# Kernel tuning notes

Hardware: AMD Instinct MI355X
Metric: run time of the kernel (lower is better)

Reference implementation:

```python
import jax, jax.numpy as jnp
import numpy as np

N_NODES = 50000
N_EDGES = 800000
D = 64
N_GRAPHS = 64


def setup_inputs() -> dict:
    key = jax.random.key(0)
    ks = jax.random.split(key, 8)
    scale = 1.0 / np.sqrt(D)
    x = jax.random.normal(ks[0], (N_NODES, D), dtype=jnp.float32)
    edge_index = jax.random.randint(ks[1], (2, N_EDGES), 0, N_NODES, dtype=jnp.int32)
    batch = jnp.sort(jax.random.randint(ks[2], (N_NODES,), 0, N_GRAPHS, dtype=jnp.int32))
    Wq = jax.random.normal(ks[3], (D, D), dtype=jnp.float32) * scale
    Wk = jax.random.normal(ks[4], (D, D), dtype=jnp.float32) * scale
    Wv = jax.random.normal(ks[5], (D, D), dtype=jnp.float32) * scale
    Ws = jax.random.normal(ks[6], (D, D), dtype=jnp.float32) * scale
    z = jnp.zeros((D,), dtype=jnp.float32)
    return {"x": x, "edge_index": edge_index, "batch": batch,
            "Wq": Wq, "bq": z, "Wk": Wk, "bk": z, "Wv": Wv, "bv": z,
            "Ws": Ws, "bs": z}


def reference(x, edge_index, batch, Wq, bq, Wk, bk, Wv, bv, Ws, bs):
    # TransformerConv(heads=1, concat=True, root_weight=True), then ReLU, then global_mean_pool
    src = edge_index[0]  # source node j (message sender)
    dst = edge_index[1]  # target node i (message receiver)
    q = x @ Wq + bq      # [N, D]
    k = x @ Wk + bk      # [N, D]
    v = x @ Wv + bv      # [N, D]
    inv_sqrt_d = jnp.float32(1.0 / np.sqrt(D))
    # per-edge attention logits: (q_i . k_j) / sqrt(D)
    logits = jnp.sum(q[dst] * k[src], axis=-1) * inv_sqrt_d  # [E]
    # segment softmax over incoming edges of each target node
    seg_max = jax.ops.segment_max(logits, dst, num_segments=N_NODES)  # [N]
    ex = jnp.exp(logits - seg_max[dst])                               # [E]
    denom = jax.ops.segment_sum(ex, dst, num_segments=N_NODES)        # [N]
    alpha = ex / denom[dst]                                           # [E]
    # scatter-add weighted values to target nodes
    agg = jax.ops.segment_sum(alpha[:, None] * v[src], dst, num_segments=N_NODES)  # [N, D]
    out = agg + (x @ Ws + bs)  # root/skip connection
    out = jax.nn.relu(out)
    # global mean pool per graph
    sums = jax.ops.segment_sum(out, batch, num_segments=N_GRAPHS)            # [G, D]
    cnt = jax.ops.segment_sum(jnp.ones((N_NODES,), out.dtype), batch, num_segments=N_GRAPHS)
    return sums / jnp.maximum(cnt, 1.0)[:, None]
```

## Files before the change

kernel.cpp:

```cpp
#include <hip/hip_runtime.h>
#include <hip/hip_bf16.h>

#define D 64
#define NG 64
#define CAP 64
#define NB 196
#define BCAP 5120

typedef short bf16x8 __attribute__((ext_vector_type(8)));
typedef float f32x4  __attribute__((ext_vector_type(4)));
typedef unsigned short u16x8 __attribute__((ext_vector_type(8)));

__device__ __forceinline__ float b2f(unsigned short u){
  return __uint_as_float(((unsigned)u) << 16);
}
__device__ __forceinline__ unsigned short f2bu(float f){
  return __builtin_bit_cast(unsigned short, __float2bfloat16(f));
}

template<int C>
__device__ __forceinline__ float dppadd(float x){
  int t = __builtin_amdgcn_update_dpp(0, __float_as_int(x), C, 0xf, 0xf, true);
  return x + __int_as_float(t);
}

__global__ __launch_bounds__(256) void k_wprep(
    const float* __restrict__ Wq, const float* __restrict__ Wk,
    const float* __restrict__ Wv, const float* __restrict__ Ws,
    short* __restrict__ fragw, int* __restrict__ zptr, int zn)
{
  for (int i = blockIdx.x*256 + threadIdx.x; i < zn; i += 8*256) zptr[i] = 0;

  const int m    = blockIdx.x >> 1;
  const int kh   = blockIdx.x & 1;
  const int ct   = threadIdx.x >> 6;
  const int lane = threadIdx.x & 63;
  const int r16  = lane & 15;
  const int kg   = lane >> 4;
  const float* Wm = (m==0) ? Wq : (m==1) ? Wk : (m==2) ? Wv : Ws;
  bf16x8 hi, lo;
  #pragma unroll
  for (int j = 0; j < 8; ++j){
    float wv = Wm[(32*kh + 8*kg + j)*D + 16*ct + r16];
    unsigned short hb = f2bu(wv);
    hi[j] = (short)hb;
    lo[j] = (short)f2bu(wv - b2f(hb));
  }
  int fi = ct*2 + kh;
  *(bf16x8*)(fragw + ((size_t)(fi*2+0)*256 + m*64 + lane)*8) = hi;
  *(bf16x8*)(fragw + ((size_t)(fi*2+1)*256 + m*64 + lane)*8) = lo;
}

__global__ __launch_bounds__(256) void k_split(
    const int* __restrict__ esrc, const int* __restrict__ edst,
    int* __restrict__ bcnt, unsigned* __restrict__ bedge, int E, int nChunk)
{
  __shared__ int hist[NB], gpos[NB], cur[NB];
  const int tid = threadIdx.x;
  if (tid < NB){ hist[tid] = 0; cur[tid] = 0; }
  __syncthreads();
  const int c0 = blockIdx.x * nChunk;
  const int c1 = min(c0 + nChunk, E);
  for (int e = c0 + tid; e < c1; e += 256)
    atomicAdd(&hist[edst[e] >> 8], 1);
  __syncthreads();
  if (tid < NB && hist[tid] > 0)
    gpos[tid] = atomicAdd(bcnt + tid*16, hist[tid]);
  __syncthreads();
  for (int e = c0 + tid; e < c1; e += 256){
    int d = edst[e];
    int b = d >> 8;
    int p = gpos[b] + atomicAdd(&cur[b], 1);
    if (p < BCAP)
      bedge[(size_t)b*BCAP + p] = (unsigned)esrc[e] | ((unsigned)(d & 255) << 16);
  }
}

__global__ __launch_bounds__(256) void k_bsort(
    const int* __restrict__ bcnt, const unsigned* __restrict__ bedge,
    int* __restrict__ cnt, unsigned short* __restrict__ slots, int N)
{
  __shared__ int cur[256];
  const int tid = threadIdx.x;
  const int b = blockIdx.x;
  cur[tid] = 0;
  __syncthreads();
  const int n = min(bcnt[b*16], BCAP);
  for (int i = tid; i < n; i += 256){
    unsigned e = bedge[(size_t)b*BCAP + i];
    int dl = e >> 16;
    int p = atomicAdd(&cur[dl], 1);
    if (p < CAP) slots[(size_t)(b*256 + dl)*CAP + p] = (unsigned short)(e & 0xFFFF);
  }
  __syncthreads();
  int dst = b*256 + tid;
  if (dst < N) cnt[dst] = cur[tid];
}

__global__ __launch_bounds__(256) void k_linear4(
    const float* __restrict__ x, const short* __restrict__ fragw,
    const float* __restrict__ bq, const float* __restrict__ bk,
    const float* __restrict__ bv, const float* __restrict__ bs,
    float* __restrict__ q, __hip_bfloat16* __restrict__ kb,
    __hip_bfloat16* __restrict__ vb, float* __restrict__ sp, int N)
{
  const int lane = threadIdx.x & 63;
  const int w    = threadIdx.x >> 6;
  const int r16  = lane & 15;
  const int kg   = lane >> 4;

  const float* bm = (w==0) ? bq : (w==1) ? bk : (w==2) ? bv : bs;

  bf16x8 wh[4][2], wl[4][2];
  #pragma unroll
  for (int fi = 0; fi < 8; ++fi){
    wh[fi>>1][fi&1] = *(const bf16x8*)(fragw + ((size_t)(fi*2+0)*256 + w*64 + lane)*8);
    wl[fi>>1][fi&1] = *(const bf16x8*)(fragw + ((size_t)(fi*2+1)*256 + w*64 + lane)*8);
  }

  const int R0 = blockIdx.x << 4;
  const float* xp = x + (size_t)(R0 + r16)*D + 8*kg;
  float4 a0 = *(const float4*)(xp);
  float4 a1 = *(const float4*)(xp + 4);
  float4 a2 = *(const float4*)(xp + 32);
  float4 a3 = *(const float4*)(xp + 36);

  bf16x8 xh[2], xl[2];
  {
    float t;
    unsigned short hb;
    #define PK(kh, j, val) t=(val); hb=f2bu(t); xh[kh][j]=(short)hb; \
                           xl[kh][j]=(short)f2bu(t - b2f(hb));
    PK(0,0,a0.x) PK(0,1,a0.y) PK(0,2,a0.z) PK(0,3,a0.w)
    PK(0,4,a1.x) PK(0,5,a1.y) PK(0,6,a1.z) PK(0,7,a1.w)
    PK(1,0,a2.x) PK(1,1,a2.y) PK(1,2,a2.z) PK(1,3,a2.w)
    PK(1,4,a3.x) PK(1,5,a3.y) PK(1,6,a3.z) PK(1,7,a3.w)
    #undef PK
  }

  #pragma unroll
  for (int ct = 0; ct < 4; ++ct){
    float bv_ = bm[16*ct + r16];
    f32x4 acc = {bv_, bv_, bv_, bv_};
    #pragma unroll
    for (int kh = 0; kh < 2; ++kh){
      acc = __builtin_amdgcn_mfma_f32_16x16x32_bf16(xh[kh], wh[ct][kh], acc, 0,0,0);
      acc = __builtin_amdgcn_mfma_f32_16x16x32_bf16(xh[kh], wl[ct][kh], acc, 0,0,0);
      acc = __builtin_amdgcn_mfma_f32_16x16x32_bf16(xl[kh], wh[ct][kh], acc, 0,0,0);
    }
    #pragma unroll
    for (int i = 0; i < 4; ++i){
      size_t o = (size_t)(R0 + 4*kg + i)*D + 16*ct + r16;
      if (w == 0)      q[o] = acc[i];
      else if (w == 1) ((unsigned short*)kb)[o] = f2bu(acc[i]);
      else if (w == 2) ((unsigned short*)vb)[o] = f2bu(acc[i]);
      else             sp[o] = acc[i];
    }
  }
}

__global__ __launch_bounds__(256) void k_attend(
    const float* __restrict__ q, const __hip_bfloat16* __restrict__ kb,
    const __hip_bfloat16* __restrict__ vb, float* __restrict__ sp,
    const int* __restrict__ cnt, const unsigned short* __restrict__ slots, int N)
{
  int node = blockIdx.x*4 + (threadIdx.x >> 6);
  if (node >= N) return;
  const int lane = threadIdx.x & 63;
  const int grp  = lane >> 3;
  const int gl   = lane & 7;

  const float4* qp = (const float4*)(q + (size_t)node*D);
  float4 qa = qp[2*gl], qb = qp[2*gl+1];

  int dg = min(cnt[node], CAP);
  int p0 = node*CAP;

  float den = 0.f;
  float4 aa = {0,0,0,0}, ab = {0,0,0,0};

  const unsigned short* ku = (const unsigned short*)kb;
  const unsigned short* vu = (const unsigned short*)vb;

  int sidx = (lane < dg) ? (int)slots[p0 + lane] : 0;
  int T = (dg + 7) >> 3;
  #pragma unroll 2
  for (int t = 0; t < T; ++t){
    int ei  = grp + 8*t;
    int eis = min(ei, dg - 1);
    int s = __shfl(sidx, eis, 64);
    if (ei < dg){
      u16x8 k8 = *(const u16x8*)(ku + (size_t)s*D + 8*gl);
      float p = qa.x*b2f(k8[0]) + qa.y*b2f(k8[1])
              + qa.z*b2f(k8[2]) + qa.w*b2f(k8[3])
              + qb.x*b2f(k8[4]) + qb.y*b2f(k8[5])
              + qb.z*b2f(k8[6]) + qb.w*b2f(k8[7]);
      p = dppadd<0xB1>(p);
      p = dppadd<0x4E>(p);
      p = dppadd<0x141>(p);
      float ex = __expf(fminf(p * 0.125f, 60.f));
      u16x8 v8 = *(const u16x8*)(vu + (size_t)s*D + 8*gl);
      den += ex;
      aa.x = fmaf(ex, b2f(v8[0]), aa.x);
      aa.y = fmaf(ex, b2f(v8[1]), aa.y);
      aa.z = fmaf(ex, b2f(v8[2]), aa.z);
      aa.w = fmaf(ex, b2f(v8[3]), aa.w);
      ab.x = fmaf(ex, b2f(v8[4]), ab.x);
      ab.y = fmaf(ex, b2f(v8[5]), ab.y);
      ab.z = fmaf(ex, b2f(v8[6]), ab.z);
      ab.w = fmaf(ex, b2f(v8[7]), ab.w);
    }
  }

  #define MRG(v) v = dppadd<0x128>(v); \
                 v += __shfl_xor(v, 16, 64); \
                 v += __shfl_xor(v, 32, 64);
  MRG(den)
  MRG(aa.x) MRG(aa.y) MRG(aa.z) MRG(aa.w)
  MRG(ab.x) MRG(ab.y) MRG(ab.z) MRG(ab.w)
  #undef MRG

  if (grp == 0){
    float4* spp = (float4*)(sp + (size_t)node*D);
    float4 s4a = spp[2*gl], s4b = spp[2*gl+1];
    float4 oa, ob;
    if (dg > 0){
      float inv = 1.f/den;
      oa.x = fmaf(aa.x, inv, s4a.x); oa.y = fmaf(aa.y, inv, s4a.y);
      oa.z = fmaf(aa.z, inv, s4a.z); oa.w = fmaf(aa.w, inv, s4a.w);
      ob.x = fmaf(ab.x, inv, s4b.x); ob.y = fmaf(ab.y, inv, s4b.y);
      ob.z = fmaf(ab.z, inv, s4b.z); ob.w = fmaf(ab.w, inv, s4b.w);
    } else {
      oa = s4a; ob = s4b;
    }
    oa.x = fmaxf(oa.x, 0.f); oa.y = fmaxf(oa.y, 0.f);
    oa.z = fmaxf(oa.z, 0.f); oa.w = fmaxf(oa.w, 0.f);
    ob.x = fmaxf(ob.x, 0.f); ob.y = fmaxf(ob.y, 0.f);
    ob.z = fmaxf(ob.z, 0.f); ob.w = fmaxf(ob.w, 0.f);
    spp[2*gl]   = oa;
    spp[2*gl+1] = ob;
  }
}

__global__ __launch_bounds__(256) void k_pool(
    const float* __restrict__ rows, const int* __restrict__ batch,
    float* __restrict__ gsum, float* __restrict__ gcnt, int N, int rpw)
{
  const int lane = threadIdx.x & 63;
  const int wid  = threadIdx.x >> 6;
  int wi = blockIdx.x*4 + wid;
  int start = wi * rpw;
  if (start >= N) return;
  int end = min(start + rpw, N);

  float acc = 0.f, c = 0.f;
  int gcur = batch[start];
  #pragma unroll 4
  for (int row = start; row < end; ++row){
    int g = batch[row];
    float val = rows[(size_t)row*D + lane];
    if (g != gcur){
      atomicAdd(gsum + (size_t)gcur*D + lane, acc);
      if (lane == 0) atomicAdd(gcnt + gcur, c);
      acc = 0.f; c = 0.f; gcur = g;
    }
    acc += val;
    c += 1.f;
  }
  atomicAdd(gsum + (size_t)gcur*D + lane, acc);
  if (lane == 0) atomicAdd(gcnt + gcur, c);
}

__global__ __launch_bounds__(256) void k_final(
    const float* __restrict__ gsum, const float* __restrict__ gcnt,
    float* __restrict__ out, int n)
{
  int i = blockIdx.x*256 + threadIdx.x;
  if (i >= n) return;
  int g = i >> 6;
  out[i] = gsum[i] / fmaxf(gcnt[g], 1.0f);
}

extern "C" void kernel_launch(void* const* d_in, const int* in_sizes, int n_in,
                              void* d_out, int out_size, void* d_ws, size_t ws_size,
                              hipStream_t stream)
{
  const float* x   = (const float*)d_in[0];
  const int*  ei   = (const int*)d_in[1];
  const int*  batch= (const int*)d_in[2];
  const float* Wq  = (const float*)d_in[3];
  const float* bq  = (const float*)d_in[4];
  const float* Wk  = (const float*)d_in[5];
  const float* bk  = (const float*)d_in[6];
  const float* Wv  = (const float*)d_in[7];
  const float* bv  = (const float*)d_in[8];
  const float* Ws  = (const float*)d_in[9];
  const float* bs  = (const float*)d_in[10];
  float* out = (float*)d_out;

  const int N = in_sizes[0] / D;
  const int E = in_sizes[1] / 2;
  const int* esrc = ei;
  const int* edst = ei + E;

  float* ws = (float*)d_ws;
  size_t off = 0;
  float* q    = ws + off; off += (size_t)N*D;
  __hip_bfloat16* kb = (__hip_bfloat16*)(ws + off); off += (size_t)N*D/2;
  __hip_bfloat16* vb = (__hip_bfloat16*)(ws + off); off += (size_t)N*D/2;
  float* sp   = ws + off; off += (size_t)N*D;
  int*   bcnt = (int*)(ws + off);  off += (size_t)NB*16;
  float* gsum = ws + off; off += (size_t)NG*D;
  float* gcnt = ws + off; off += NG;
  int*   cnt  = (int*)(ws + off);  off += N;
  unsigned* bedge = (unsigned*)(ws + off); off += (size_t)NB*BCAP;
  unsigned short* slots = (unsigned short*)(ws + off); off += (size_t)N*CAP/2;
  short* fragw = (short*)(ws + off); off += 16*256*8/2;

  const int zn = NB*16 + NG*D + NG;
  const int nChunk = (E + 255) / 256;

  k_wprep  <<<8, 256, 0, stream>>>(Wq, Wk, Wv, Ws, fragw, bcnt, zn);
  k_split  <<<256, 256, 0, stream>>>(esrc, edst, bcnt, bedge, E, nChunk);
  k_bsort  <<<NB, 256, 0, stream>>>(bcnt, bedge, cnt, slots, N);
  k_linear4<<<N/16, 256, 0, stream>>>(x, fragw, bq, bk, bv, bs,
                                      q, kb, vb, sp, N);
  k_attend <<<(N+3)/4, 256, 0, stream>>>(q, kb, vb, sp, cnt, slots, N);
  const int rpw = 32;
  int nwaves = (N + rpw - 1) / rpw;
  k_pool <<<(nwaves+3)/4, 256, 0, stream>>>(sp, batch, gsum, gcnt, N, rpw);
  k_final<<<(NG*D+255)/256, 256, 0, stream>>>(gsum, gcnt, out, NG*D);
}
```

Baseline: 113.2 us.

## Fuse edge bucketing and node linear projections into one heterogeneous launch

Merges the edge-splitting kernel and the QKV/skip linear kernel into one launch. The first 256 blocks do edge bucketing and the rest compute the projections, with each linear block now handling two 16-row strips. Both phases depend only on k_wprep, so they can run at the same time, and one kernel launch and one inter-kernel gap go away. The risks are higher register pressure from the merged kernel, which may lower occupancy, and load imbalance between the two kinds of block.

Result: faster. 102.2 us (-9.8%).

```diff
diff --git a/kernel.cpp b/kernel.cpp
--- a/kernel.cpp
+++ b/kernel.cpp
@@ -51,28 +51,101 @@
   *(bf16x8*)(fragw + ((size_t)(fi*2+1)*256 + m*64 + lane)*8) = lo;
 }
 
-__global__ __launch_bounds__(256) void k_split(
+__global__ __launch_bounds__(256) void k_fused(
     const int* __restrict__ esrc, const int* __restrict__ edst,
-    int* __restrict__ bcnt, unsigned* __restrict__ bedge, int E, int nChunk)
+    int* __restrict__ bcnt, unsigned* __restrict__ bedge, int E, int nChunk,
+    int nSplit,
+    const float* __restrict__ x, const short* __restrict__ fragw,
+    const float* __restrict__ bq, const float* __restrict__ bk,
+    const float* __restrict__ bv, const float* __restrict__ bs,
+    float* __restrict__ q, __hip_bfloat16* __restrict__ kb,
+    __hip_bfloat16* __restrict__ vb, float* __restrict__ sp, int N)
 {
   __shared__ int hist[NB], gpos[NB], cur[NB];
-  const int tid = threadIdx.x;
-  if (tid < NB){ hist[tid] = 0; cur[tid] = 0; }
-  __syncthreads();
-  const int c0 = blockIdx.x * nChunk;
-  const int c1 = min(c0 + nChunk, E);
-  for (int e = c0 + tid; e < c1; e += 256)
-    atomicAdd(&hist[edst[e] >> 8], 1);
-  __syncthreads();
-  if (tid < NB && hist[tid] > 0)
-    gpos[tid] = atomicAdd(bcnt + tid*16, hist[tid]);
-  __syncthreads();
-  for (int e = c0 + tid; e < c1; e += 256){
-    int d = edst[e];
-    int b = d >> 8;
-    int p = gpos[b] + atomicAdd(&cur[b], 1);
-    if (p < BCAP)
-      bedge[(size_t)b*BCAP + p] = (unsigned)esrc[e] | ((unsigned)(d & 255) << 16);
+
+  if ((int)blockIdx.x < nSplit){
+    const int tid = threadIdx.x;
+    if (tid < NB){ hist[tid] = 0; cur[tid] = 0; }
+    __syncthreads();
+    const int c0 = blockIdx.x * nChunk;
+    const int c1 = min(c0 + nChunk, E);
+    for (int e = c0 + tid; e < c1; e += 256)
+      atomicAdd(&hist[edst[e] >> 8], 1);
+    __syncthreads();
+    if (tid < NB && hist[tid] > 0)
+      gpos[tid] = atomicAdd(bcnt + tid*16, hist[tid]);
+    __syncthreads();
+    for (int e = c0 + tid; e < c1; e += 256){
+      int d = edst[e];
+      int b = d >> 8;
+      int p = gpos[b] + atomicAdd(&cur[b], 1);
+      if (p < BCAP)
+        bedge[(size_t)b*BCAP + p] = (unsigned)esrc[e] | ((unsigned)(d & 255) << 16);
+    }
+    return;
+  }
+
+  const int lane = threadIdx.x & 63;
+  const int w    = threadIdx.x >> 6;
+  const int r16  = lane & 15;
+  const int kg   = lane >> 4;
+
+  const float* bm = (w==0) ? bq : (w==1) ? bk : (w==2) ? bv : bs;
+
+  bf16x8 wh[4][2], wl[4][2];
+  #pragma unroll
+  for (int fi = 0; fi < 8; ++fi){
+    wh[fi>>1][fi&1] = *(const bf16x8*)(fragw + ((size_t)(fi*2+0)*256 + w*64 + lane)*8);
+    wl[fi>>1][fi&1] = *(const bf16x8*)(fragw + ((size_t)(fi*2+1)*256 + w*64 + lane)*8);
+  }
+  float bias[4];
+  #pragma unroll
+  for (int ct = 0; ct < 4; ++ct) bias[ct] = bm[16*ct + r16];
+
+  const int nStrip = N >> 4;
+  const int s0 = (blockIdx.x - nSplit) * 2;
+  #pragma unroll
+  for (int it = 0; it < 2; ++it){
+    const int strip = s0 + it;
+    if (strip >= nStrip) break;
+    const int R0 = strip << 4;
+    const float* xp = x + (size_t)(R0 + r16)*D + 8*kg;
+    float4 a0 = *(const float4*)(xp);
+    float4 a1 = *(const float4*)(xp + 4);
+    float4 a2 = *(const float4*)(xp + 32);
+    float4 a3 = *(const float4*)(xp + 36);
+
+    bf16x8 xh[2], xl[2];
+    {
+      float t;
+      unsigned short hb;
+      #define PK(kh, j, val) t=(val); hb=f2bu(t); xh[kh][j]=(short)hb; \
+                             xl[kh][j]=(short)f2bu(t - b2f(hb));
+      PK(0,0,a0.x) PK(0,1,a0.y) PK(0,2,a0.z) PK(0,3,a0.w)
+      PK(0,4,a1.x) PK(0,5,a1.y) PK(0,6,a1.z) PK(0,7,a1.w)
+      PK(1,0,a2.x) PK(1,1,a2.y) PK(1,2,a2.z) PK(1,3,a2.w)
+      PK(1,4,a3.x) PK(1,5,a3.y) PK(1,6,a3.z) PK(1,7,a3.w)
+      #undef PK
+    }
+
+    #pragma unroll
+    for (int ct = 0; ct < 4; ++ct){
+      f32x4 acc = {bias[ct], bias[ct], bias[ct], bias[ct]};
+      #pragma unroll
+      for (int kh = 0; kh < 2; ++kh){
+        acc = __builtin_amdgcn_mfma_f32_16x16x32_bf16(xh[kh], wh[ct][kh], acc, 0,0,0);
+        acc = __builtin_amdgcn_mfma_f32_16x16x32_bf16(xh[kh], wl[ct][kh], acc, 0,0,0);
+        acc = __builtin_amdgcn_mfma_f32_16x16x32_bf16(xl[kh], wh[ct][kh], acc, 0,0,0);
+      }
+      #pragma unroll
+      for (int i = 0; i < 4; ++i){
+        size_t o = (size_t)(R0 + 4*kg + i)*D + 16*ct + r16;
+        if (w == 0)      q[o] = acc[i];
+        else if (w == 1) ((unsigned short*)kb)[o] = f2bu(acc[i]);
+        else if (w == 2) ((unsigned short*)vb)[o] = f2bu(acc[i]);
+        else             sp[o] = acc[i];
+      }
+    }
   }
 }
 
@@ -95,68 +168,6 @@
   __syncthreads();
   int dst = b*256 + tid;
   if (dst < N) cnt[dst] = cur[tid];
-}
-
-__global__ __launch_bounds__(256) void k_linear4(
-    const float* __restrict__ x, const short* __restrict__ fragw,
-    const float* __restrict__ bq, const float* __restrict__ bk,
-    const float* __restrict__ bv, const float* __restrict__ bs,
-    float* __restrict__ q, __hip_bfloat16* __restrict__ kb,
-    __hip_bfloat16* __restrict__ vb, float* __restrict__ sp, int N)
-{
-  const int lane = threadIdx.x & 63;
-  const int w    = threadIdx.x >> 6;
-  const int r16  = lane & 15;
-  const int kg   = lane >> 4;
-
-  const float* bm = (w==0) ? bq : (w==1) ? bk : (w==2) ? bv : bs;
-
-  bf16x8 wh[4][2], wl[4][2];
-  #pragma unroll
-  for (int fi = 0; fi < 8; ++fi){
-    wh[fi>>1][fi&1] = *(const bf16x8*)(fragw + ((size_t)(fi*2+0)*256 + w*64 + lane)*8);
-    wl[fi>>1][fi&1] = *(const bf16x8*)(fragw + ((size_t)(fi*2+1)*256 + w*64 + lane)*8);
-  }
-
-  const int R0 = blockIdx.x << 4;
-  const float* xp = x + (size_t)(R0 + r16)*D + 8*kg;
-  float4 a0 = *(const float4*)(xp);
-  float4 a1 = *(const float4*)(xp + 4);
-  float4 a2 = *(const float4*)(xp + 32);
-  float4 a3 = *(const float4*)(xp + 36);
-
-  bf16x8 xh[2], xl[2];
-  {
-    float t;
-    unsigned short hb;
-    #define PK(kh, j, val) t=(val); hb=f2bu(t); xh[kh][j]=(short)hb; \
-                           xl[kh][j]=(short)f2bu(t - b2f(hb));
-    PK(0,0,a0.x) PK(0,1,a0.y) PK(0,2,a0.z) PK(0,3,a0.w)
-    PK(0,4,a1.x) PK(0,5,a1.y) PK(0,6,a1.z) PK(0,7,a1.w)
-    PK(1,0,a2.x) PK(1,1,a2.y) PK(1,2,a2.z) PK(1,3,a2.w)
-    PK(1,4,a3.x) PK(1,5,a3.y) PK(1,6,a3.z) PK(1,7,a3.w)
-    #undef PK
-  }
-
-  #pragma unroll
-  for (int ct = 0; ct < 4; ++ct){
-    float bv_ = bm[16*ct + r16];
-    f32x4 acc = {bv_, bv_, bv_, bv_};
-    #pragma unroll
-    for (int kh = 0; kh < 2; ++kh){
-      acc = __builtin_amdgcn_mfma_f32_16x16x32_bf16(xh[kh], wh[ct][kh], acc, 0,0,0);
-      acc = __builtin_amdgcn_mfma_f32_16x16x32_bf16(xh[kh], wl[ct][kh], acc, 0,0,0);
-      acc = __builtin_amdgcn_mfma_f32_16x16x32_bf16(xl[kh], wh[ct][kh], acc, 0,0,0);
-    }
-    #pragma unroll
-    for (int i = 0; i < 4; ++i){
-      size_t o = (size_t)(R0 + 4*kg + i)*D + 16*ct + r16;
-      if (w == 0)      q[o] = acc[i];
-      else if (w == 1) ((unsigned short*)kb)[o] = f2bu(acc[i]);
-      else if (w == 2) ((unsigned short*)vb)[o] = f2bu(acc[i]);
-      else             sp[o] = acc[i];
-    }
-  }
 }
 
 __global__ __launch_bounds__(256) void k_attend(
@@ -319,13 +330,15 @@
 
   const int zn = NB*16 + NG*D + NG;
   const int nChunk = (E + 255) / 256;
-
-  k_wprep  <<<8, 256, 0, stream>>>(Wq, Wk, Wv, Ws, fragw, bcnt, zn);
-  k_split  <<<256, 256, 0, stream>>>(esrc, edst, bcnt, bedge, E, nChunk);
-  k_bsort  <<<NB, 256, 0, stream>>>(bcnt, bedge, cnt, slots, N);
-  k_linear4<<<N/16, 256, 0, stream>>>(x, fragw, bq, bk, bv, bs,
-                                      q, kb, vb, sp, N);
-  k_attend <<<(N+3)/4, 256, 0, stream>>>(q, kb, vb, sp, cnt, slots, N);
+  const int nSplit = 256;
+  const int nLin   = ((N >> 4) + 1) / 2;
+
+  k_wprep <<<8, 256, 0, stream>>>(Wq, Wk, Wv, Ws, fragw, bcnt, zn);
+  k_fused <<<nSplit + nLin, 256, 0, stream>>>(esrc, edst, bcnt, bedge, E, nChunk,
+                                              nSplit, x, fragw, bq, bk, bv, bs,
+                                              q, kb, vb, sp, N);
+  k_bsort <<<NB, 256, 0, stream>>>(bcnt, bedge, cnt, slots, N);
+  k_attend<<<(N+3)/4, 256, 0, stream>>>(q, kb, vb, sp, cnt, slots, N);
   const int rpw = 32;
   int nwaves = (N + rpw - 1) / rpw;
   k_pool <<<(nwaves+3)/4, 256, 0, stream>>>(sp, batch, gsum, gcnt, N, rpw);
```
